# Optimization experiments

Hardware: AMD Instinct MI355X
Metric: run time of the kernel (lower is better)

Reference implementation:

```python
import jax, jax.numpy as jnp
import numpy as np

B, T, C = 4, 2048, 1024


def setup_inputs() -> dict:
    key = jax.random.key(0)
    ks = jax.random.split(key, 5)
    s = 1.0 / np.sqrt(C)
    return {
        "X": jax.random.normal(ks[0], (B, T, C), dtype=jnp.float32),
        "Wq": jax.random.normal(ks[1], (C, C), dtype=jnp.float32) * s,
        "Wk": jax.random.normal(ks[2], (C, C), dtype=jnp.float32) * s,
        "Wv": jax.random.normal(ks[3], (C, C), dtype=jnp.float32) * s,
        "Wo": jax.random.normal(ks[4], (C, C), dtype=jnp.float32) * s,
    }


def reference(X, Wq, Wk, Wv, Wo):
    Bx, Tx, Cx = X.shape
    Q = X @ Wq  # [B,T,C]
    K = X @ Wk
    V = X @ Wv
    scores = jnp.einsum('btc,bsc->bts', Q, K) / jnp.sqrt(jnp.asarray(Cx, X.dtype))
    # causal mask: position t attends to s <= t
    causal = jnp.tril(jnp.ones((Tx, Tx), dtype=bool))
    scores = jnp.where(causal, scores, jnp.asarray(-jnp.inf, scores.dtype))
    weights = jax.nn.softmax(scores, axis=-1)
    out = jnp.einsum('bts,bsc->btc', weights, V)
    return out @ Wo
```

## Files before the change

### kernel.cpp

```cpp
#include <hip/hip_runtime.h>
#include <hip/hip_bf16.h>
#include <cmath>


typedef __attribute__((ext_vector_type(8))) __bf16 bf16x8;
typedef __attribute__((ext_vector_type(8))) short short8;
typedef __attribute__((ext_vector_type(4))) float f32x4;

__device__ __forceinline__ unsigned short f2bf(float f) {
  union { float f; unsigned u; } v; v.f = f;
  unsigned u = v.u;
  u += ((u >> 16) & 1u) + 0x7fffu;
  return (unsigned short)(u >> 16);
}
__device__ __forceinline__ float bf2f(unsigned short h) {
  union { unsigned u; float f; } v; v.u = ((unsigned)h) << 16;
  return v.f;
}

#define GLDS(gp, sp)                                                           \
  __builtin_amdgcn_global_load_lds(                                            \
      (const __attribute__((address_space(1))) void*)(gp),                     \
      (__attribute__((address_space(3))) void*)(sp), 16, 0, 0)

__global__ void prep(const float* __restrict__ X,
                     const float* __restrict__ w0, const float* __restrict__ w1,
                     const float* __restrict__ w2, const float* __restrict__ w3,
                     unsigned short* __restrict__ Xb,
                     unsigned short* __restrict__ wcat,
                     unsigned short* __restrict__ wvb,
                     unsigned short* __restrict__ wot,
                     int n) {
  if (blockIdx.z == 2) {
    int bx = blockIdx.x * 32, by = blockIdx.y * 32;
    int tx = threadIdx.x, ty = threadIdx.y;
#pragma unroll
    for (int i = 0; i < 32; i += 8) {
      size_t idx = (size_t)(by + ty + i) * n + bx + tx;
      wvb[idx] = f2bf(w2[idx]);
    }
  } else if (blockIdx.z < 4) {
    const float* src = blockIdx.z == 0 ? w0 : blockIdx.z == 1 ? w1 : w3;
    unsigned short* dst = blockIdx.z == 0 ? wcat
                          : blockIdx.z == 1 ? wcat + (size_t)n * n : wot;
    __shared__ float tile[32][33];
    int bx = blockIdx.x * 32, by = blockIdx.y * 32;
    int tx = threadIdx.x, ty = threadIdx.y;
#pragma unroll
    for (int i = 0; i < 32; i += 8)
      tile[ty + i][tx] = src[(size_t)(by + ty + i) * n + bx + tx];
    __syncthreads();
#pragma unroll
    for (int i = 0; i < 32; i += 8)
      dst[(size_t)(bx + ty + i) * n + by + tx] = f2bf(tile[tx][ty + i]);
  } else {
    const int bid = (blockIdx.z - 4) * 1024 + blockIdx.y * 32 + blockIdx.x;
    const int t = threadIdx.y * 32 + threadIdx.x;
    const int i = (bid * 256 + t) * 4;
    float4 f = *(const float4*)(X + i);
    ushort4 o = make_ushort4(f2bf(f.x), f2bf(f.y), f2bf(f.z), f2bf(f.w));
    *(ushort4*)(Xb + i) = o;
  }
}

template <typename OutT, int NW>
__global__ __launch_bounds__(NW * 64, NW / 2)
void gemm_bt(const unsigned short* __restrict__ A, int lda, long long sA,
             const unsigned short* __restrict__ B, int ldb, long long sB,
             OutT* __restrict__ Cp, int ldc, long long sC,
             int K, float alpha, int tri, int kcap, int gx) {
  A  += (long long)blockIdx.z * sA;
  B  += (long long)blockIdx.z * sB;
  Cp += (long long)blockIdx.z * sC;

  int by, bx;
  if (tri) {
    const int idx = blockIdx.x;
    by = (int)((sqrtf(8.f * idx + 1.f) - 1.f) * 0.5f);
    while (by * (by + 1) / 2 > idx) --by;
    while ((by + 1) * (by + 2) / 2 <= idx) ++by;
    bx = idx - by * (by + 1) / 2;
  } else if (gx > 0) {
    const int id = blockIdx.x;
    const int gs = gx * 8;
    const int g = id / gs, r = id - g * gs;
    bx = r >> 3;
    by = g * 8 + (r & 7);
    if (kcap) by = (gridDim.x / gx) - 1 - by;
  } else {
    by = blockIdx.y;
    bx = blockIdx.x;
  }
  const int m0 = by * 128;
  const int n0 = bx * 128;
  const int Keff = kcap ? min(K, m0 + 128) : K;

  const int tid  = threadIdx.x;
  const int lane = tid & 63;
  const int w    = tid >> 6;
  const int wm   = (NW == 4) ? (w >> 1) * 64 : (w >> 1) * 32;
  const int wn   = (w & 1) * 64;
  const int quad = lane >> 4;
  const int l16  = lane & 15;
  constexpr int AI = (NW == 4) ? 4 : 2;
  constexpr int NR = 128 / (NW * 8);

  __shared__ unsigned short As[8192];
  __shared__ unsigned short Bs[8192];

  f32x4 acc[AI][4];
#pragma unroll
  for (int i = 0; i < AI; ++i)
#pragma unroll
    for (int j = 0; j < 4; ++j)
      acc[i][j] = (f32x4){0.f, 0.f, 0.f, 0.f};

  const int srow = tid >> 3;
  const int scol = ((tid & 7) ^ (srow & 7)) * 8;
  const unsigned short* gA = A + (long long)(m0 + srow) * lda + scol;
  const unsigned short* gB = B + (long long)(n0 + srow) * ldb + scol;
  const int rsw = l16 & 7;

  for (int kt = 0; kt < Keff; kt += 64) {
    __syncthreads();
#pragma unroll
    for (int r = 0; r < NR; ++r) {
      GLDS(gA + (long long)(r * NW * 8) * lda + kt, As + r * NW * 512 + tid * 8);
      GLDS(gB + (long long)(r * NW * 8) * ldb + kt, Bs + r * NW * 512 + tid * 8);
    }
    __syncthreads();
#pragma unroll
    for (int ks = 0; ks < 2; ++ks) {
      bf16x8 af[AI], bfr[4];
#pragma unroll
      for (int i = 0; i < AI; ++i)
        af[i] = *(const bf16x8*)(As + (wm + i * 16 + l16) * 64 +
                                 ((ks * 4 + quad) ^ rsw) * 8);
#pragma unroll
      for (int j = 0; j < 4; ++j)
        bfr[j] = *(const bf16x8*)(Bs + (wn + j * 16 + l16) * 64 +
                                  ((ks * 4 + quad) ^ rsw) * 8);
#pragma unroll
      for (int i = 0; i < AI; ++i)
#pragma unroll
        for (int j = 0; j < 4; ++j)
          acc[i][j] = __builtin_amdgcn_mfma_f32_16x16x32_bf16(af[i], bfr[j],
                                                              acc[i][j], 0, 0, 0);
    }
  }

#pragma unroll
  for (int i = 0; i < AI; ++i) {
#pragma unroll
    for (int j = 0; j < 4; ++j) {
      const int row = m0 + wm + i * 16 + quad * 4;
      const int col = n0 + wn + j * 16 + l16;
#pragma unroll
      for (int r = 0; r < 4; ++r) {
        float v = acc[i][j][r] * alpha;
        if constexpr (sizeof(OutT) == 2)
          Cp[(long long)(row + r) * ldc + col] = (OutT)f2bf(v);
        else
          Cp[(long long)(row + r) * ldc + col] = v;
      }
    }
  }
}

__global__ __launch_bounds__(256, 2)
void gemm_qkv(const unsigned short* __restrict__ A, int lda,
              const unsigned short* __restrict__ B, int ldb,
              unsigned short* __restrict__ Cp, int K, int gx) {
  const int id = blockIdx.x;
  const int gs = gx * 8;
  const int g = id / gs, r = id - g * gs;
  const int bx = r >> 3;
  const int by = g * 8 + (r & 7);
  const int m0 = by * 128;
  const int n0 = bx * 128;

  const int tid  = threadIdx.x;
  const int lane = tid & 63;
  const int w    = tid >> 6;
  const int wm   = (w >> 1) * 64;
  const int wn   = (w & 1) * 64;
  const int quad = lane >> 4;
  const int l16  = lane & 15;

  __shared__ unsigned short As[8192];
  __shared__ unsigned short Bs[8192];

  f32x4 acc[4][4];
#pragma unroll
  for (int i = 0; i < 4; ++i)
#pragma unroll
    for (int j = 0; j < 4; ++j)
      acc[i][j] = (f32x4){0.f, 0.f, 0.f, 0.f};

  const int srow = tid >> 3;
  const int scol = ((tid & 7) ^ (srow & 7)) * 8;
  const unsigned short* gA = A + (long long)(m0 + srow) * lda + scol;
  const unsigned short* gB = B + (long long)(n0 + srow) * ldb + scol;
  const int rsw = l16 & 7;

  for (int kt = 0; kt < K; kt += 64) {
    __syncthreads();
#pragma unroll
    for (int r2 = 0; r2 < 4; ++r2) {
      GLDS(gA + (long long)(r2 * 32) * lda + kt, As + r2 * 2048 + tid * 8);
      GLDS(gB + (long long)(r2 * 32) * ldb + kt, Bs + r2 * 2048 + tid * 8);
    }
    __syncthreads();
#pragma unroll
    for (int ks = 0; ks < 2; ++ks) {
      bf16x8 af[4], bfr[4];
#pragma unroll
      for (int i = 0; i < 4; ++i)
        af[i] = *(const bf16x8*)(As + (wm + i * 16 + l16) * 64 +
                                 ((ks * 4 + quad) ^ rsw) * 8);
#pragma unroll
      for (int j = 0; j < 4; ++j)
        bfr[j] = *(const bf16x8*)(Bs + (wn + j * 16 + l16) * 64 +
                                  ((ks * 4 + quad) ^ rsw) * 8);
#pragma unroll
      for (int i = 0; i < 4; ++i)
#pragma unroll
        for (int j = 0; j < 4; ++j)
          acc[i][j] = __builtin_amdgcn_mfma_f32_16x16x32_bf16(af[i], bfr[j],
                                                              acc[i][j], 0, 0, 0);
    }
  }

#pragma unroll
  for (int i = 0; i < 4; ++i) {
#pragma unroll
    for (int j = 0; j < 4; ++j) {
      const int row = m0 + wm + i * 16 + quad * 4;
      const int col = n0 + wn + j * 16 + l16;
      if (col >= 2048) {
        const int b = row >> 11, t = row & 2047, cv = col - 2048;
        ushort4 o = make_ushort4(f2bf(acc[i][j][0]), f2bf(acc[i][j][1]),
                                 f2bf(acc[i][j][2]), f2bf(acc[i][j][3]));
        *(ushort4*)(Cp + 16777216LL + ((long long)(b * 1024 + cv)) * 2048 + t) = o;
      } else {
        unsigned short* dst = Cp + (col >= 1024 ? 8388608LL - 1024 : 0);
#pragma unroll
        for (int r2 = 0; r2 < 4; ++r2)
          dst[(long long)(row + r2) * 1024 + col] = f2bf(acc[i][j][r2]);
      }
    }
  }
}

__global__ __launch_bounds__(256)
void softmax_causal(unsigned short* __restrict__ S, int T) {
  const long long row = blockIdx.x;
  const int t = (int)(row & (long long)(T - 1));
  const int limit = ((t >> 7) + 1) << 7;
  unsigned short* p = S + row * T;
  const int tid  = threadIdx.x;
  const int base = tid * 8;
  const bool active = base < limit;

  short8 raw = {};
  if (active) raw = *(const short8*)(p + base);
  float x[8];
  float mx = -1e30f;
#pragma unroll
  for (int j = 0; j < 8; ++j) {
    bool valid = active && (base + j) <= t;
    x[j] = valid ? bf2f((unsigned short)raw[j]) : -1e30f;
    mx = fmaxf(mx, x[j]);
  }
#pragma unroll
  for (int off = 32; off > 0; off >>= 1) mx = fmaxf(mx, __shfl_xor(mx, off));
  __shared__ float red[8];
  const int wv = tid >> 6;
  if ((tid & 63) == 0) red[wv] = mx;
  __syncthreads();
  mx = fmaxf(fmaxf(red[0], red[1]), fmaxf(red[2], red[3]));

  float sum = 0.f;
#pragma unroll
  for (int j = 0; j < 8; ++j) {
    bool valid = active && (base + j) <= t;
    x[j] = valid ? __expf(x[j] - mx) : 0.f;
    sum += x[j];
  }
#pragma unroll
  for (int off = 32; off > 0; off >>= 1) sum += __shfl_xor(sum, off);
  if ((tid & 63) == 0) red[4 + wv] = sum;
  __syncthreads();
  sum = red[4] + red[5] + red[6] + red[7];
  const float inv = 1.f / sum;

  if (active) {
    unsigned short out[8];
#pragma unroll
    for (int j = 0; j < 8; ++j) out[j] = f2bf(x[j] * inv);
    *(short8*)(p + base) = *(const short8*)out;
  }
}

extern "C" void kernel_launch(void* const* d_in, const int* in_sizes, int n_in,
                              void* d_out, int out_size, void* d_ws,
                              size_t ws_size, hipStream_t stream) {
  (void)in_sizes; (void)n_in; (void)out_size; (void)ws_size;
  const int Bb = 4, T = 2048, C = 1024;
  const int M = Bb * T;

  const float* X  = (const float*)d_in[0];
  const float* Wq = (const float*)d_in[1];
  const float* Wk = (const float*)d_in[2];
  const float* Wv = (const float*)d_in[3];
  const float* Wo = (const float*)d_in[4];
  float* Out = (float*)d_out;

  char* w = (char*)d_ws;
  unsigned short* Wcat = (unsigned short*)w; w += (size_t)3 * C * C * 2;
  unsigned short* Q    = (unsigned short*)w; w += (size_t)M * C * 2;
  unsigned short* Kb   = (unsigned short*)w; w += (size_t)M * C * 2;
  unsigned short* Vt   = (unsigned short*)w; w += (size_t)M * C * 2;
  unsigned short* Xb   = (unsigned short*)w; w += (size_t)M * C * 2;
  unsigned short* Wvb  = (unsigned short*)d_out;
  unsigned short* Wot  = (unsigned short*)d_out + (size_t)C * C;
  unsigned short* S    = (unsigned short*)d_out;
  float*          OutT = (float*)Q;

  prep<<<dim3(32, 32, 12), dim3(32, 8), 0, stream>>>(X, Wq, Wk, Wv, Wo, Xb,
                                                     Wcat, Wvb, Wot, C);

  gemm_bt<unsigned short, 4><<<dim3(C / 128, C / 128, 1), dim3(256), 0, stream>>>(
      Wot, C, 0, Wvb, C, 0, Wcat + (size_t)2 * C * C, C, 0, C, 1.f, 0, 0, 0);

  gemm_qkv<<<dim3((3 * C / 128) * (M / 128)), dim3(256), 0, stream>>>(
      Xb, C, Wcat, C, Q, C, 3 * C / 128);

  const int ntri = (T / 128) * (T / 128 + 1) / 2;
  gemm_bt<unsigned short, 8><<<dim3(ntri, 1, Bb), dim3(512), 0, stream>>>(
      Q, C, (long long)T * C, Kb, C, (long long)T * C,
      S, T, (long long)T * T, C, 0.03125f, 1, 0, 0);

  softmax_causal<<<M, 256, 0, stream>>>(S, T);

  gemm_bt<float, 8><<<dim3((C / 128) * (T / 128), 1, Bb), dim3(512), 0, stream>>>(
      S, T, (long long)T * T, Vt, T, (long long)C * T,
      OutT, C, (long long)T * C, T, 1.f, 0, 1, C / 128);

  hipMemcpyAsync(Out, OutT, (size_t)M * C * sizeof(float),
                 hipMemcpyDeviceToDevice, stream);
}
```

Measured before the change: 273.6 us.

## Pipeline QKV GEMM with 256x256 double-buffered tiles and drop output memcpy

Replaces the QKV projection GEMM with a 512-thread, 256x256-tile kernel. It double-buffers 128KB of dynamic LDS, issues global-to-LDS loads in phases interleaved with MFMA groups, and uses explicit waitcnt, barriers and setprio. Softmax now writes into the Q buffer instead of in place, so the final PV GEMM can write straight into the output and the device-to-device memcpy goes away. The risks are lower occupancy from the large LDS footprint, a fragile hand-written schedule, and a grid swizzle that assumes the block count is divisible by 8.

```diff
diff --git a/kernel.cpp b/kernel.cpp
--- a/kernel.cpp
+++ b/kernel.cpp
@@ -167,72 +167,125 @@
   }
 }
 
-__global__ __launch_bounds__(256, 2)
-void gemm_qkv(const unsigned short* __restrict__ A, int lda,
-              const unsigned short* __restrict__ B, int ldb,
-              unsigned short* __restrict__ Cp, int K, int gx) {
-  const int id = blockIdx.x;
-  const int gs = gx * 8;
-  const int g = id / gs, r = id - g * gs;
-  const int bx = r >> 3;
-  const int by = g * 8 + (r & 7);
-  const int m0 = by * 128;
-  const int n0 = bx * 128;
+
+#define STG(tt, st, bb) do {                                                  \
+    const int ld_ = (st) < 2 ? lda : ldb;                                     \
+    const unsigned short* gp_ = ((st) < 2 ? gA : gB)                          \
+        + (long long)(((st) & 1) * 128) * ld_ + (long long)(tt) * 64;         \
+    unsigned short* sp_ = smem + ((bb) << 15) + (((st) >= 2) ? 16384 : 0)     \
+        + (((st) & 1) * 128) * 64 + tid * 8;                                  \
+    GLDS(gp_, sp_);                                                           \
+    GLDS(gp_ + (long long)64 * ld_, sp_ + 4096);                              \
+  } while (0)
+
+#define LDA_PH(mh)                                                            \
+  _Pragma("unroll") for (int i = 0; i < 4; ++i)                               \
+  _Pragma("unroll") for (int ks = 0; ks < 2; ++ks)                            \
+    bA[i][ks] = *(const bf16x8*)(Ab + (wm + (mh) * 64 + i * 16 + l16) * 64 +  \
+                                 (((ks * 4 + quad) ^ rsw) * 8));
+
+#define LDB_PH(j0)                                                            \
+  _Pragma("unroll") for (int j = 0; j < 2; ++j)                               \
+  _Pragma("unroll") for (int ks = 0; ks < 2; ++ks)                            \
+    bB[(j0) + j][ks] = *(const bf16x8*)(Bb + (wn + ((j0) + j) * 16 + l16) * 64\
+                                        + (((ks * 4 + quad) ^ rsw) * 8));
+
+#define MM(mh, j0)                                                            \
+  _Pragma("unroll") for (int i = 0; i < 4; ++i)                               \
+  _Pragma("unroll") for (int j = 0; j < 2; ++j)                               \
+  _Pragma("unroll") for (int ks = 0; ks < 2; ++ks)                            \
+    acc[(mh) * 4 + i][(j0) + j] = __builtin_amdgcn_mfma_f32_16x16x32_bf16(    \
+        bA[i][ks], bB[(j0) + j][ks], acc[(mh) * 4 + i][(j0) + j], 0, 0, 0);
+
+#define PHASE_SYNC()                                                          \
+  __builtin_amdgcn_s_barrier();                                               \
+  asm volatile("s_waitcnt lgkmcnt(0)" ::: "memory");                          \
+  __builtin_amdgcn_sched_barrier(0);
+
+#define GROUP(T_, B_) do {                                                    \
+    const unsigned short* Ab = smem + ((B_) << 15);                           \
+    const unsigned short* Bb = Ab + 16384;                                    \
+                                                                      \
+    LDA_PH(0); LDB_PH(0);                                                     \
+    if ((T_) + 1 < nt) STG((T_) + 1, 1, (B_) ^ 1);                            \
+    asm volatile("s_waitcnt lgkmcnt(8)" ::: "memory");                        \
+    PHASE_SYNC();                                                             \
+    __builtin_amdgcn_s_setprio(1); MM(0, 0); __builtin_amdgcn_s_setprio(0);   \
+    __builtin_amdgcn_s_barrier();                                             \
+                                                                      \
+    LDB_PH(2);                                                                \
+    if ((T_) + 1 < nt) STG((T_) + 1, 2, (B_) ^ 1);                            \
+    PHASE_SYNC();                                                             \
+    __builtin_amdgcn_s_setprio(1); MM(0, 2); __builtin_amdgcn_s_setprio(0);   \
+    __builtin_amdgcn_s_barrier();                                             \
+                                                                      \
+    LDA_PH(1);                                                                \
+    if ((T_) + 1 < nt) STG((T_) + 1, 3, (B_) ^ 1);                            \
+    PHASE_SYNC();                                                             \
+    __builtin_amdgcn_s_setprio(1); MM(1, 2); __builtin_amdgcn_s_setprio(0);   \
+    __builtin_amdgcn_s_barrier();                                             \
+                                                                      \
+    if ((T_) + 2 < nt) {                                                      \
+      STG((T_) + 2, 0, (B_));                                                 \
+      asm volatile("s_waitcnt vmcnt(2)" ::: "memory");                        \
+    } else {                                                                  \
+      asm volatile("s_waitcnt vmcnt(0)" ::: "memory");                        \
+    }                                                                         \
+    __builtin_amdgcn_s_barrier();                                             \
+    __builtin_amdgcn_s_setprio(1); MM(1, 0); __builtin_amdgcn_s_setprio(0);   \
+    __builtin_amdgcn_s_barrier();                                             \
+  } while (0)
+
+__global__ __launch_bounds__(512, 2)
+void gemm_qkv8(const unsigned short* __restrict__ A, int lda,
+               const unsigned short* __restrict__ B, int ldb,
+               unsigned short* __restrict__ Cp, int K) {
+  const int id  = blockIdx.x;
+  const int cpx = gridDim.x >> 3;
+  const int sw  = (id & 7) * cpx + (id >> 3);
+  const int bx  = sw % 12;
+  const int by  = sw / 12;
+  const int m0  = by * 256;
+  const int n0  = bx * 256;
 
   const int tid  = threadIdx.x;
   const int lane = tid & 63;
   const int w    = tid >> 6;
-  const int wm   = (w >> 1) * 64;
-  const int wn   = (w & 1) * 64;
+  const int wm   = (w >> 2) * 128;
+  const int wn   = (w & 3) * 64;
   const int quad = lane >> 4;
   const int l16  = lane & 15;
-
-  __shared__ unsigned short As[8192];
-  __shared__ unsigned short Bs[8192];
-
-  f32x4 acc[4][4];
-#pragma unroll
-  for (int i = 0; i < 4; ++i)
-#pragma unroll
-    for (int j = 0; j < 4; ++j)
-      acc[i][j] = (f32x4){0.f, 0.f, 0.f, 0.f};
+  const int rsw  = l16 & 7;
+
+  extern __shared__ unsigned short smem[];
 
   const int srow = tid >> 3;
   const int scol = ((tid & 7) ^ (srow & 7)) * 8;
   const unsigned short* gA = A + (long long)(m0 + srow) * lda + scol;
   const unsigned short* gB = B + (long long)(n0 + srow) * ldb + scol;
-  const int rsw = l16 & 7;
-
-  for (int kt = 0; kt < K; kt += 64) {
-    __syncthreads();
-#pragma unroll
-    for (int r2 = 0; r2 < 4; ++r2) {
-      GLDS(gA + (long long)(r2 * 32) * lda + kt, As + r2 * 2048 + tid * 8);
-      GLDS(gB + (long long)(r2 * 32) * ldb + kt, Bs + r2 * 2048 + tid * 8);
-    }
-    __syncthreads();
-#pragma unroll
-    for (int ks = 0; ks < 2; ++ks) {
-      bf16x8 af[4], bfr[4];
-#pragma unroll
-      for (int i = 0; i < 4; ++i)
-        af[i] = *(const bf16x8*)(As + (wm + i * 16 + l16) * 64 +
-                                 ((ks * 4 + quad) ^ rsw) * 8);
-#pragma unroll
-      for (int j = 0; j < 4; ++j)
-        bfr[j] = *(const bf16x8*)(Bs + (wn + j * 16 + l16) * 64 +
-                                  ((ks * 4 + quad) ^ rsw) * 8);
-#pragma unroll
-      for (int i = 0; i < 4; ++i)
-#pragma unroll
-        for (int j = 0; j < 4; ++j)
-          acc[i][j] = __builtin_amdgcn_mfma_f32_16x16x32_bf16(af[i], bfr[j],
-                                                              acc[i][j], 0, 0, 0);
-    }
-  }
-
-#pragma unroll
-  for (int i = 0; i < 4; ++i) {
+
+  f32x4 acc[8][4];
+#pragma unroll
+  for (int i = 0; i < 8; ++i)
+#pragma unroll
+    for (int j = 0; j < 4; ++j)
+      acc[i][j] = (f32x4){0.f, 0.f, 0.f, 0.f};
+
+  bf16x8 bA[4][2], bB[4][2];
+  const int nt = K >> 6;
+
+  STG(0, 0, 0); STG(0, 1, 0); STG(0, 2, 0); STG(0, 3, 0);
+  STG(1, 0, 1);
+  asm volatile("s_waitcnt vmcnt(2)" ::: "memory");
+  __builtin_amdgcn_s_barrier();
+
+  for (int tt = 0; tt < nt; tt += 2) {
+    GROUP(tt, 0);
+    GROUP(tt + 1, 1);
+  }
+
+#pragma unroll
+  for (int i = 0; i < 8; ++i) {
 #pragma unroll
     for (int j = 0; j < 4; ++j) {
       const int row = m0 + wm + i * 16 + quad * 4;
@@ -252,18 +305,27 @@
   }
 }
 
+#undef GROUP
+#undef PHASE_SYNC
+#undef MM
+#undef LDB_PH
+#undef LDA_PH
+#undef STG
+
 __global__ __launch_bounds__(256)
-void softmax_causal(unsigned short* __restrict__ S, int T) {
+void softmax_causal(const unsigned short* __restrict__ Sin,
+                    unsigned short* __restrict__ Sout, int T) {
   const long long row = blockIdx.x;
   const int t = (int)(row & (long long)(T - 1));
   const int limit = ((t >> 7) + 1) << 7;
-  unsigned short* p = S + row * T;
+  const unsigned short* pin = Sin + row * T;
+  unsigned short* pout = Sout + row * T;
   const int tid  = threadIdx.x;
   const int base = tid * 8;
   const bool active = base < limit;
 
   short8 raw = {};
-  if (active) raw = *(const short8*)(p + base);
+  if (active) raw = *(const short8*)(pin + base);
   float x[8];
   float mx = -1e30f;
 #pragma unroll
@@ -298,7 +360,7 @@
     unsigned short out[8];
 #pragma unroll
     for (int j = 0; j < 8; ++j) out[j] = f2bf(x[j] * inv);
-    *(short8*)(p + base) = *(const short8*)out;
+    *(short8*)(pout + base) = *(const short8*)out;
   }
 }
 
@@ -314,7 +376,6 @@
   const float* Wk = (const float*)d_in[2];
   const float* Wv = (const float*)d_in[3];
   const float* Wo = (const float*)d_in[4];
-  float* Out = (float*)d_out;
 
   char* w = (char*)d_ws;
   unsigned short* Wcat = (unsigned short*)w; w += (size_t)3 * C * C * 2;
@@ -322,10 +383,18 @@
   unsigned short* Kb   = (unsigned short*)w; w += (size_t)M * C * 2;
   unsigned short* Vt   = (unsigned short*)w; w += (size_t)M * C * 2;
   unsigned short* Xb   = (unsigned short*)w; w += (size_t)M * C * 2;
+  (void)Kb;
   unsigned short* Wvb  = (unsigned short*)d_out;
   unsigned short* Wot  = (unsigned short*)d_out + (size_t)C * C;
   unsigned short* S    = (unsigned short*)d_out;
-  float*          OutT = (float*)Q;
+  unsigned short* Sn   = Q;
+
+  static int smem_set = 0;
+  if (!smem_set) {
+    hipFuncSetAttribute(reinterpret_cast<const void*>(gemm_qkv8),
+                        hipFuncAttributeMaxDynamicSharedMemorySize, 131072);
+    smem_set = 1;
+  }
 
   prep<<<dim3(32, 32, 12), dim3(32, 8), 0, stream>>>(X, Wq, Wk, Wv, Wo, Xb,
                                                      Wcat, Wvb, Wot, C);
@@ -333,20 +402,17 @@
   gemm_bt<unsigned short, 4><<<dim3(C / 128, C / 128, 1), dim3(256), 0, stream>>>(
       Wot, C, 0, Wvb, C, 0, Wcat + (size_t)2 * C * C, C, 0, C, 1.f, 0, 0, 0);
 
-  gemm_qkv<<<dim3((3 * C / 128) * (M / 128)), dim3(256), 0, stream>>>(
-      Xb, C, Wcat, C, Q, C, 3 * C / 128);
+  gemm_qkv8<<<dim3((M / 256) * (3 * C / 256)), dim3(512), 131072, stream>>>(
+      Xb, C, Wcat, C, Q, C);
 
   const int ntri = (T / 128) * (T / 128 + 1) / 2;
   gemm_bt<unsigned short, 8><<<dim3(ntri, 1, Bb), dim3(512), 0, stream>>>(
       Q, C, (long long)T * C, Kb, C, (long long)T * C,
       S, T, (long long)T * T, C, 0.03125f, 1, 0, 0);
 
-  softmax_causal<<<M, 256, 0, stream>>>(S, T);
+  softmax_causal<<<M, 256, 0, stream>>>(S, Sn, T);
 
   gemm_bt<float, 8><<<dim3((C / 128) * (T / 128), 1, Bb), dim3(512), 0, stream>>>(
-      S, T, (long long)T * T, Vt, T, (long long)C * T,
-      OutT, C, (long long)T * C, T, 1.f, 0, 1, C / 128);
-
-  hipMemcpyAsync(Out, OutT, (size_t)M * C * sizeof(float),
-                 hipMemcpyDeviceToDevice, stream);
-}
+      Sn, T, (long long)T * T, Vt, T, (long long)C * T,
+      (float*)d_out, C, (long long)T * C, T, 1.f, 0, 1, C / 128);
+}
```

New measurement: 269.0 us. Within noise of the previous version (-1.7%).
